# Performance work log

Hardware: AMD Instinct MI355X
Metric: run time of the kernel (lower is better)

Reference implementation:

```python
import jax, jax.numpy as jnp
import numpy as np

LEAKY_SLOPE = 0.2  # tf.nn.leaky_relu default alpha
NEG_INF = -1e9


def setup_inputs() -> dict:
    key = jax.random.key(0)
    k1, k2, k3, k4 = jax.random.split(key, 4)
    B, N, F, D, H = 1, 4096, 128, 64, 4
    features = jax.random.normal(k1, (B, N, F), dtype=jnp.float32)
    adj = jax.random.randint(k2, (N, N), 0, 2, dtype=jnp.int32)  # 0/1 adjacency
    W = jax.random.normal(k3, (H, F, D), dtype=jnp.float32) * 0.1
    attn_k = jax.random.normal(k4, (H, 2 * D, 1), dtype=jnp.float32) * 0.1
    return {"adj": adj, "features": features, "W": W, "attn_k": attn_k}


def reference(adj, features, W, attn_k):
    H, _, D = W.shape
    adj_f = adj.astype(jnp.float32)[None]       # [1, N, N], broadcast over batch
    mask = adj_f != 0.0
    outs = []
    for i in range(H):  # fixed small head loop (heads are structurally distinct weights)
        h = features @ W[i]                      # [B, N, D]
        a_self = h @ attn_k[i, :D]               # [B, N, 1]
        a_neigh = h @ attn_k[i, D:]              # [B, N, 1]
        scores = a_self + jnp.swapaxes(a_neigh, 1, 2)  # [B, N, N] additive scores
        scores = jax.nn.leaky_relu(scores, LEAKY_SLOPE)
        scores = jnp.where(mask, scores, NEG_INF)
        attn = jax.nn.softmax(scores, axis=-1)   # [B, N, N]
        outs.append((attn * adj_f) @ h)          # [B, N, D]
    out = jnp.concatenate(outs, axis=-1) if H > 1 else outs[0]
    return jax.nn.relu(out)
```

## Files before the change

kernel.cpp:

```cpp
#include <hip/hip_runtime.h>
#include <math.h>

#define NN 4096
#define FF 128
#define DD 64
#define HH 4
#define NC 256

typedef _Float16 f16x8 __attribute__((ext_vector_type(8)));
typedef _Float16 f16x2 __attribute__((ext_vector_type(2)));
typedef float    f32x4 __attribute__((ext_vector_type(4)));

__global__ __launch_bounds__(256) void adjbits_kernel(
    const int* __restrict__ adj, unsigned int* __restrict__ adjw)
{
    const int row  = blockIdx.x;
    const int wv   = threadIdx.x >> 6;
    const int lane = threadIdx.x & 63;
    for (int c = wv; c < 64; c += 4) {
        int a = adj[(size_t)row * NN + c * 64 + lane];
        unsigned long long m = __ballot(a != 0);
        if (lane == 0) {
            adjw[row * 128 + c * 2]     = (unsigned int)m;
            adjw[row * 128 + c * 2 + 1] = (unsigned int)(m >> 32);
        }
    }
}

__global__ __launch_bounds__(256) void prep_kernel(
    const float* __restrict__ feats, const float* __restrict__ W,
    const float* __restrict__ ak, _Float16* __restrict__ Ht,
    _Float16* __restrict__ Es, _Float16* __restrict__ Fs,
    _Float16* __restrict__ En, _Float16* __restrict__ Fn)
{
    __shared__ float Wt[64 * 132];
    __shared__ float ft[32 * 128];
    __shared__ float hlds[32 * 65];
    const int t  = threadIdx.x;
    const int h  = blockIdx.y;
    const int n0 = blockIdx.x * 32;

    {
        const float* Wh = W + h * (FF * DD);
        #pragma unroll
        for (int j = 0; j < 8; ++j) {
            int idx = j * 256 + t;
            int f   = idx >> 4;
            int d4  = idx & 15;
            float4 v = ((const float4*)Wh)[idx];
            Wt[(d4 * 4 + 0) * 132 + f] = v.x;
            Wt[(d4 * 4 + 1) * 132 + f] = v.y;
            Wt[(d4 * 4 + 2) * 132 + f] = v.z;
            Wt[(d4 * 4 + 3) * 132 + f] = v.w;
        }
        #pragma unroll
        for (int j = 0; j < 4; ++j) {
            int idx = j * 256 + t;
            int r = idx >> 5, f4 = idx & 31;
            ((float4*)ft)[r * 32 + f4] = ((const float4*)feats)[(size_t)(n0 + r) * 32 + f4];
        }
    }
    __syncthreads();

    const int d   = t & 63;
    const int wid = t >> 6;
    float acc[8];
    #pragma unroll
    for (int j = 0; j < 8; ++j) acc[j] = 0.f;

    for (int f4 = 0; f4 < 32; ++f4) {
        const float4 w4 = *(const float4*)&Wt[d * 132 + f4 * 4];
        #pragma unroll
        for (int j = 0; j < 8; ++j) {
            const int r = wid + 4 * j;
            const float4 fv = *(const float4*)&ft[r * 128 + f4 * 4];
            acc[j] += fv.x * w4.x + fv.y * w4.y + fv.z * w4.z + fv.w * w4.w;
        }
    }

    const float aks = ak[h * 128 + d];
    const float akn = ak[h * 128 + 64 + d];
    #pragma unroll
    for (int j = 0; j < 8; ++j) {
        const int r = wid + 4 * j;
        const float hv = acc[j];
        hlds[r * 65 + d] = hv;
        float v1 = hv * aks;
        float v2 = hv * akn;
        #pragma unroll
        for (int m = 32; m >= 1; m >>= 1) {
            v1 += __shfl_xor(v1, m, 64);
            v2 += __shfl_xor(v2, m, 64);
        }
        if (d == 0) {
            Es[h * NN + n0 + r] = (_Float16)__expf(v1);
            Fs[h * NN + n0 + r] = (_Float16)__expf(0.2f * v1);
            En[h * NN + n0 + r] = (_Float16)__expf(v2);
            Fn[h * NN + n0 + r] = (_Float16)__expf(0.2f * v2);
        }
    }
    __syncthreads();

    const int d2 = t >> 2;
    const int mq = (t & 3) * 8;
    f16x8 v;
    #pragma unroll
    for (int i = 0; i < 8; ++i) v[i] = (_Float16)hlds[(mq + i) * 65 + d2];
    *(f16x8*)(Ht + (size_t)(h * 64 + d2) * NN + n0 + mq) = v;
}

__global__ __launch_bounds__(256, 4) void attn_kernel(
    const unsigned int* __restrict__ adjw, const _Float16* __restrict__ Ht,
    const _Float16* __restrict__ Es, const _Float16* __restrict__ Fs,
    const _Float16* __restrict__ En, const _Float16* __restrict__ Fn,
    float* __restrict__ pacc, float* __restrict__ pden, int ksplit)
{
    __shared__ _Float16 Blds[2 * 64 * 32];

    const int t  = threadIdx.x;
    const int w  = t >> 6;
    const int l  = t & 63;
    const int lr = l & 15;
    const int kg = l >> 4;
    const int h  = blockIdx.y;
    const int s  = blockIdx.z;
    const int n0 = blockIdx.x * 128 + w * 32;
    const int mstart = s * ksplit;
    const int nchunk = ksplit >> 5;

    const int sd = t >> 2;
    const int sg = (t & 3) ^ (sd & 3);
    const _Float16* __restrict__ hstage = Ht + (size_t)(h * 64 + sd) * NN + sg * 8;
    const int swoff = sd * 32 + (t & 3) * 8;
    const int slot8 = (kg ^ (lr & 3)) * 8;

    const _Float16 es0 = Es[h * NN + n0 + lr],      fs0 = Fs[h * NN + n0 + lr];
    const _Float16 es1 = Es[h * NN + n0 + 16 + lr], fs1 = Fs[h * NN + n0 + 16 + lr];
    const f16x2 es20 = {es0, es0}, fs20 = {fs0, fs0};
    const f16x2 es21 = {es1, es1}, fs21 = {fs1, fs1};

    const _Float16* __restrict__ EnB = En + (size_t)h * NN;
    const _Float16* __restrict__ FnB = Fn + (size_t)h * NN;
    const int row0 = n0 + lr, row1 = n0 + 16 + lr;
    const int wb   = mstart >> 5;

    f32x4 acc[2][4] = {};
    f32x4 dacc[2]   = {};
    f16x8 ones;
    #pragma unroll
    for (int j = 0; j < 8; ++j) ones[j] = (_Float16)1.0f;

    union U8 { f16x8 v; unsigned int u[4]; };

    uint4 sreg = *(const uint4*)(hstage + mstart);

    for (int cq = 0; cq < (nchunk >> 2); ++cq) {
        const uint4 mk0 = *(const uint4*)&adjw[(size_t)row0 * 128 + wb + cq * 4];
        const uint4 mk1 = *(const uint4*)&adjw[(size_t)row1 * 128 + wb + cq * 4];

        #pragma unroll
        for (int ci = 0; ci < 4; ++ci) {
            const int c  = cq * 4 + ci;
            const int m0 = mstart + c * 32;
            const int buf = (ci & 1) * 2048;

            *(uint4*)&Blds[buf + swoff] = sreg;
            __syncthreads();

            {
                const int mn = (c + 1 < nchunk) ? m0 + 32 : m0;
                sreg = *(const uint4*)(hstage + mn);
            }

            const uint4 enq = *(const uint4*)(EnB + m0 + kg * 8);
            const uint4 fnq = *(const uint4*)(FnB + m0 + kg * 8);
            const unsigned int b0 =
                (ci == 0 ? mk0.x : ci == 1 ? mk0.y : ci == 2 ? mk0.z : mk0.w) >> (kg * 8);
            const unsigned int b1 =
                (ci == 0 ? mk1.x : ci == 1 ? mk1.y : ci == 2 ? mk1.z : mk1.w) >> (kg * 8);

            U8 A0, A1;
            #pragma unroll
            for (int p = 0; p < 4; ++p) {
                const unsigned int eu = p == 0 ? enq.x : p == 1 ? enq.y : p == 2 ? enq.z : enq.w;
                const unsigned int fu = p == 0 ? fnq.x : p == 1 ? fnq.y : p == 2 ? fnq.z : fnq.w;
                const f16x2 en2 = __builtin_bit_cast(f16x2, eu);
                const f16x2 fn2 = __builtin_bit_cast(f16x2, fu);
                const f16x2 v0 = __builtin_elementwise_max(es20 * en2, fs20 * fn2);
                const f16x2 v1 = __builtin_elementwise_max(es21 * en2, fs21 * fn2);
                const unsigned int mm0 = (((b0 >> (2 * p)) & 1u) ? 0x0000FFFFu : 0u)
                                       | (((b0 >> (2 * p + 1)) & 1u) ? 0xFFFF0000u : 0u);
                const unsigned int mm1 = (((b1 >> (2 * p)) & 1u) ? 0x0000FFFFu : 0u)
                                       | (((b1 >> (2 * p + 1)) & 1u) ? 0xFFFF0000u : 0u);
                A0.u[p] = __builtin_bit_cast(unsigned int, v0) & mm0;
                A1.u[p] = __builtin_bit_cast(unsigned int, v1) & mm1;
            }

            #pragma unroll
            for (int cb = 0; cb < 4; ++cb) {
                const f16x8 Bf = *(const f16x8*)&Blds[buf + (cb * 16 + lr) * 32 + slot8];
                acc[0][cb] = __builtin_amdgcn_mfma_f32_16x16x32_f16(A0.v, Bf, acc[0][cb], 0, 0, 0);
                acc[1][cb] = __builtin_amdgcn_mfma_f32_16x16x32_f16(A1.v, Bf, acc[1][cb], 0, 0, 0);
            }
            dacc[0] = __builtin_amdgcn_mfma_f32_16x16x32_f16(A0.v, ones, dacc[0], 0, 0, 0);
            dacc[1] = __builtin_amdgcn_mfma_f32_16x16x32_f16(A1.v, ones, dacc[1], 0, 0, 0);

            __syncthreads();
        }
    }

    #pragma unroll
    for (int rb = 0; rb < 2; ++rb) {
        #pragma unroll
        for (int r = 0; r < 4; ++r) {
            const int row = n0 + rb * 16 + kg * 4 + r;
            #pragma unroll
            for (int cb = 0; cb < 4; ++cb)
                pacc[((size_t)(s * NN + row)) * NC + h * 64 + cb * 16 + lr] = acc[rb][cb][r];
            if (lr == 0)
                pden[(s * NN + row) * 4 + h] = dacc[rb][r];
        }
    }
}

__global__ __launch_bounds__(256) void finalize_kernel(
    const float* __restrict__ pacc, const float* __restrict__ pden,
    float* __restrict__ out, int nsplit)
{
    const int n = blockIdx.x;
    const int c = threadIdx.x;
    float a = 0.f, d = 0.f;
    for (int s = 0; s < nsplit; ++s) {
        a += pacc[((size_t)(s * NN + n)) * NC + c];
        d += pden[(s * NN + n) * 4 + (c >> 6)];
    }
    const float o = (d > 0.f) ? a / d : 0.f;
    out[(size_t)n * NC + c] = o > 0.f ? o : 0.f;
}

extern "C" void kernel_launch(void* const* d_in, const int* in_sizes, int n_in,
                              void* d_out, int out_size, void* d_ws, size_t ws_size,
                              hipStream_t stream)
{
    const int*   adj   = (const int*)d_in[0];
    const float* feats = (const float*)d_in[1];
    const float* W     = (const float*)d_in[2];
    const float* ak    = (const float*)d_in[3];
    float*       out   = (float*)d_out;

    char* ws = (char*)d_ws;
    unsigned int* adjw = (unsigned int*)ws;
    _Float16*     Ht   = (_Float16*)(ws + (2ull << 20));
    _Float16*     Es   = (_Float16*)(ws + (4ull << 20));
    _Float16*     Fs   = (_Float16*)(ws + (4ull << 20) + (1 << 16));
    _Float16*     En   = (_Float16*)(ws + (4ull << 20) + (2 << 16));
    _Float16*     Fn   = (_Float16*)(ws + (4ull << 20) + (3 << 16));
    float*        pden = (float*)(ws + (4ull << 20) + (4 << 16));
    float*        pacc = (float*)(ws + (5ull << 20));

    int nsplit = 8;
    while (nsplit > 1 && ws_size < (5ull << 20) + (size_t)nsplit * (4ull << 20))
        nsplit >>= 1;
    const int ksplit = NN / nsplit;

    adjbits_kernel<<<NN, 256, 0, stream>>>(adj, adjw);
    prep_kernel<<<dim3(128, 4), 256, 0, stream>>>(feats, W, ak, Ht, Es, Fs, En, Fn);
    attn_kernel<<<dim3(32, 4, nsplit), 256, 0, stream>>>(adjw, Ht, Es, Fs, En, Fn, pacc, pden, ksplit);
    finalize_kernel<<<NN, 256, 0, stream>>>(pacc, pden, out, nsplit);
}
```

Baseline: 67.34 us.

## Pre-pack H in MFMA fragment layout and load B directly into registers

The prep kernel now writes H in a pre-swizzled per-32-row-chunk layout that matches the MFMA B-operand fragment, so the attention kernel can load B straight from global memory into registers. This removes the shared-memory staging and both __syncthreads per chunk. Each block is now a single wavefront, and B fragments are double-buffered in registers by software prefetch. The change also raises MFMA issue priority around the math and uses nontemporal stores for the partial sums, at the cost of more register pressure and each wave fetching B on its own rather than sharing it through LDS.

Result: slower. 70.25 us (+4.3%).

```diff
diff --git a/kernel.cpp b/kernel.cpp
--- a/kernel.cpp
+++ b/kernel.cpp
@@ -29,7 +29,7 @@
 
 __global__ __launch_bounds__(256) void prep_kernel(
     const float* __restrict__ feats, const float* __restrict__ W,
-    const float* __restrict__ ak, _Float16* __restrict__ Ht,
+    const float* __restrict__ ak, _Float16* __restrict__ Bpack,
     _Float16* __restrict__ Es, _Float16* __restrict__ Fs,
     _Float16* __restrict__ En, _Float16* __restrict__ Fn)
 {
@@ -101,38 +101,33 @@
     }
     __syncthreads();
 
-    const int d2 = t >> 2;
-    const int mq = (t & 3) * 8;
+    const int cb = t >> 6;
+    const int l  = t & 63;
+    const int lr = l & 15;
+    const int kg = l >> 4;
     f16x8 v;
     #pragma unroll
-    for (int i = 0; i < 8; ++i) v[i] = (_Float16)hlds[(mq + i) * 65 + d2];
-    *(f16x8*)(Ht + (size_t)(h * 64 + d2) * NN + n0 + mq) = v;
-}
-
-__global__ __launch_bounds__(256, 4) void attn_kernel(
-    const unsigned int* __restrict__ adjw, const _Float16* __restrict__ Ht,
+    for (int j = 0; j < 8; ++j)
+        v[j] = (_Float16)hlds[(kg * 8 + j) * 65 + cb * 16 + lr];
+    *(f16x8*)(Bpack + ((size_t)(h * 128 + blockIdx.x)) * 2048 + (cb * 64 + l) * 8) = v;
+}
+
+__global__ __launch_bounds__(64, 4) void attn_kernel(
+    const unsigned int* __restrict__ adjw, const _Float16* __restrict__ Bpack,
     const _Float16* __restrict__ Es, const _Float16* __restrict__ Fs,
     const _Float16* __restrict__ En, const _Float16* __restrict__ Fn,
     float* __restrict__ pacc, float* __restrict__ pden, int ksplit)
 {
-    __shared__ _Float16 Blds[2 * 64 * 32];
-
-    const int t  = threadIdx.x;
-    const int w  = t >> 6;
-    const int l  = t & 63;
+    const int l  = threadIdx.x;
     const int lr = l & 15;
     const int kg = l >> 4;
     const int h  = blockIdx.y;
+    const int n0 = blockIdx.x * 32;
     const int s  = blockIdx.z;
-    const int n0 = blockIdx.x * 128 + w * 32;
+
     const int mstart = s * ksplit;
     const int nchunk = ksplit >> 5;
-
-    const int sd = t >> 2;
-    const int sg = (t & 3) ^ (sd & 3);
-    const _Float16* __restrict__ hstage = Ht + (size_t)(h * 64 + sd) * NN + sg * 8;
-    const int swoff = sd * 32 + (t & 3) * 8;
-    const int slot8 = (kg ^ (lr & 3)) * 8;
+    const int wb     = mstart >> 5;
 
     const _Float16 es0 = Es[h * NN + n0 + lr],      fs0 = Fs[h * NN + n0 + lr];
     const _Float16 es1 = Es[h * NN + n0 + 16 + lr], fs1 = Fs[h * NN + n0 + 16 + lr];
@@ -142,7 +137,9 @@
     const _Float16* __restrict__ EnB = En + (size_t)h * NN;
     const _Float16* __restrict__ FnB = Fn + (size_t)h * NN;
     const int row0 = n0 + lr, row1 = n0 + 16 + lr;
-    const int wb   = mstart >> 5;
+
+    const _Float16* __restrict__ bp =
+        Bpack + ((size_t)(h * 128) + (mstart >> 5)) * 2048 + l * 8;
 
     f32x4 acc[2][4] = {};
     f32x4 dacc[2]   = {};
@@ -152,62 +149,67 @@
 
     union U8 { f16x8 v; unsigned int u[4]; };
 
-    uint4 sreg = *(const uint4*)(hstage + mstart);
+    f16x8 B_0[4], B_1[4];
+
+#define LOADB(DST, CIDX) do {                                                 \
+        int _c = (CIDX); _c = _c < nchunk ? _c : nchunk - 1;                  \
+        const _Float16* _b = bp + (size_t)_c * 2048;                          \
+        _Pragma("unroll")                                                     \
+        for (int _cb = 0; _cb < 4; ++_cb)                                     \
+            DST[_cb] = *(const f16x8*)(_b + _cb * 512);                       \
+    } while (0)
+
+#define STEP(BREG, C, MW0, MW1) do {                                          \
+        const int _m0 = mstart + (C) * 32;                                    \
+        const uint4 enq = *(const uint4*)(EnB + _m0 + kg * 8);                \
+        const uint4 fnq = *(const uint4*)(FnB + _m0 + kg * 8);                \
+        const unsigned int b0 = (MW0) >> (kg * 8);                            \
+        const unsigned int b1 = (MW1) >> (kg * 8);                            \
+        U8 A0, A1;                                                            \
+        _Pragma("unroll")                                                     \
+        for (int p = 0; p < 4; ++p) {                                         \
+            const unsigned int eu = p == 0 ? enq.x : p == 1 ? enq.y : p == 2 ? enq.z : enq.w; \
+            const unsigned int fu = p == 0 ? fnq.x : p == 1 ? fnq.y : p == 2 ? fnq.z : fnq.w; \
+            const f16x2 en2 = __builtin_bit_cast(f16x2, eu);                  \
+            const f16x2 fn2 = __builtin_bit_cast(f16x2, fu);                  \
+            const f16x2 v0 = __builtin_elementwise_max(es20 * en2, fs20 * fn2); \
+            const f16x2 v1 = __builtin_elementwise_max(es21 * en2, fs21 * fn2); \
+            const unsigned int mm0 = (((b0 >> (2 * p)) & 1u) ? 0x0000FFFFu : 0u) \
+                                   | (((b0 >> (2 * p + 1)) & 1u) ? 0xFFFF0000u : 0u); \
+            const unsigned int mm1 = (((b1 >> (2 * p)) & 1u) ? 0x0000FFFFu : 0u) \
+                                   | (((b1 >> (2 * p + 1)) & 1u) ? 0xFFFF0000u : 0u); \
+            A0.u[p] = __builtin_bit_cast(unsigned int, v0) & mm0;             \
+            A1.u[p] = __builtin_bit_cast(unsigned int, v1) & mm1;             \
+        }                                                                     \
+        __builtin_amdgcn_s_setprio(1);                                        \
+        _Pragma("unroll")                                                     \
+        for (int _cb = 0; _cb < 4; ++_cb) {                                   \
+            acc[0][_cb] = __builtin_amdgcn_mfma_f32_16x16x32_f16(A0.v, BREG[_cb], acc[0][_cb], 0, 0, 0); \
+            acc[1][_cb] = __builtin_amdgcn_mfma_f32_16x16x32_f16(A1.v, BREG[_cb], acc[1][_cb], 0, 0, 0); \
+        }                                                                     \
+        dacc[0] = __builtin_amdgcn_mfma_f32_16x16x32_f16(A0.v, ones, dacc[0], 0, 0, 0); \
+        dacc[1] = __builtin_amdgcn_mfma_f32_16x16x32_f16(A1.v, ones, dacc[1], 0, 0, 0); \
+        __builtin_amdgcn_s_setprio(0);                                        \
+    } while (0)
+
+    LOADB(B_0, 0);
 
     for (int cq = 0; cq < (nchunk >> 2); ++cq) {
-        const uint4 mk0 = *(const uint4*)&adjw[(size_t)row0 * 128 + wb + cq * 4];
-        const uint4 mk1 = *(const uint4*)&adjw[(size_t)row1 * 128 + wb + cq * 4];
-
-        #pragma unroll
-        for (int ci = 0; ci < 4; ++ci) {
-            const int c  = cq * 4 + ci;
-            const int m0 = mstart + c * 32;
-            const int buf = (ci & 1) * 2048;
-
-            *(uint4*)&Blds[buf + swoff] = sreg;
-            __syncthreads();
-
-            {
-                const int mn = (c + 1 < nchunk) ? m0 + 32 : m0;
-                sreg = *(const uint4*)(hstage + mn);
-            }
-
-            const uint4 enq = *(const uint4*)(EnB + m0 + kg * 8);
-            const uint4 fnq = *(const uint4*)(FnB + m0 + kg * 8);
-            const unsigned int b0 =
-                (ci == 0 ? mk0.x : ci == 1 ? mk0.y : ci == 2 ? mk0.z : mk0.w) >> (kg * 8);
-            const unsigned int b1 =
-                (ci == 0 ? mk1.x : ci == 1 ? mk1.y : ci == 2 ? mk1.z : mk1.w) >> (kg * 8);
-
-            U8 A0, A1;
-            #pragma unroll
-            for (int p = 0; p < 4; ++p) {
-                const unsigned int eu = p == 0 ? enq.x : p == 1 ? enq.y : p == 2 ? enq.z : enq.w;
-                const unsigned int fu = p == 0 ? fnq.x : p == 1 ? fnq.y : p == 2 ? fnq.z : fnq.w;
-                const f16x2 en2 = __builtin_bit_cast(f16x2, eu);
-                const f16x2 fn2 = __builtin_bit_cast(f16x2, fu);
-                const f16x2 v0 = __builtin_elementwise_max(es20 * en2, fs20 * fn2);
-                const f16x2 v1 = __builtin_elementwise_max(es21 * en2, fs21 * fn2);
-                const unsigned int mm0 = (((b0 >> (2 * p)) & 1u) ? 0x0000FFFFu : 0u)
-                                       | (((b0 >> (2 * p + 1)) & 1u) ? 0xFFFF0000u : 0u);
-                const unsigned int mm1 = (((b1 >> (2 * p)) & 1u) ? 0x0000FFFFu : 0u)
-                                       | (((b1 >> (2 * p + 1)) & 1u) ? 0xFFFF0000u : 0u);
-                A0.u[p] = __builtin_bit_cast(unsigned int, v0) & mm0;
-                A1.u[p] = __builtin_bit_cast(unsigned int, v1) & mm1;
-            }
-
-            #pragma unroll
-            for (int cb = 0; cb < 4; ++cb) {
-                const f16x8 Bf = *(const f16x8*)&Blds[buf + (cb * 16 + lr) * 32 + slot8];
-                acc[0][cb] = __builtin_amdgcn_mfma_f32_16x16x32_f16(A0.v, Bf, acc[0][cb], 0, 0, 0);
-                acc[1][cb] = __builtin_amdgcn_mfma_f32_16x16x32_f16(A1.v, Bf, acc[1][cb], 0, 0, 0);
-            }
-            dacc[0] = __builtin_amdgcn_mfma_f32_16x16x32_f16(A0.v, ones, dacc[0], 0, 0, 0);
-            dacc[1] = __builtin_amdgcn_mfma_f32_16x16x32_f16(A1.v, ones, dacc[1], 0, 0, 0);
-
-            __syncthreads();
-        }
-    }
+        const int c0 = cq * 4;
+        const uint4 mk0 = *(const uint4*)&adjw[(size_t)row0 * 128 + wb + c0];
+        const uint4 mk1 = *(const uint4*)&adjw[(size_t)row1 * 128 + wb + c0];
+
+        LOADB(B_1, c0 + 1);
+        STEP(B_0, c0 + 0, mk0.x, mk1.x);
+        LOADB(B_0, c0 + 2);
+        STEP(B_1, c0 + 1, mk0.y, mk1.y);
+        LOADB(B_1, c0 + 3);
+        STEP(B_0, c0 + 2, mk0.z, mk1.z);
+        LOADB(B_0, c0 + 4);
+        STEP(B_1, c0 + 3, mk0.w, mk1.w);
+    }
+#undef LOADB
+#undef STEP
 
     #pragma unroll
     for (int rb = 0; rb < 2; ++rb) {
@@ -215,8 +217,11 @@
         for (int r = 0; r < 4; ++r) {
             const int row = n0 + rb * 16 + kg * 4 + r;
             #pragma unroll
-            for (int cb = 0; cb < 4; ++cb)
-                pacc[((size_t)(s * NN + row)) * NC + h * 64 + cb * 16 + lr] = acc[rb][cb][r];
+            for (int cb = 0; cb < 4; ++cb) {
+                float4 vv = {acc[rb][cb][r], 0.f, 0.f, 0.f};
+                __builtin_nontemporal_store(acc[rb][cb][r],
+                    &pacc[((size_t)(s * NN + row)) * NC + h * 64 + cb * 16 + lr]);
+            }
             if (lr == 0)
                 pden[(s * NN + row) * 4 + h] = dacc[rb][r];
         }
@@ -249,14 +254,14 @@
     float*       out   = (float*)d_out;
 
     char* ws = (char*)d_ws;
-    unsigned int* adjw = (unsigned int*)ws;
-    _Float16*     Ht   = (_Float16*)(ws + (2ull << 20));
-    _Float16*     Es   = (_Float16*)(ws + (4ull << 20));
-    _Float16*     Fs   = (_Float16*)(ws + (4ull << 20) + (1 << 16));
-    _Float16*     En   = (_Float16*)(ws + (4ull << 20) + (2 << 16));
-    _Float16*     Fn   = (_Float16*)(ws + (4ull << 20) + (3 << 16));
-    float*        pden = (float*)(ws + (4ull << 20) + (4 << 16));
-    float*        pacc = (float*)(ws + (5ull << 20));
+    unsigned int* adjw  = (unsigned int*)ws;
+    _Float16*     Bpack = (_Float16*)(ws + (2ull << 20));
+    _Float16*     Es    = (_Float16*)(ws + (4ull << 20));
+    _Float16*     Fs    = (_Float16*)(ws + (4ull << 20) + (1 << 16));
+    _Float16*     En    = (_Float16*)(ws + (4ull << 20) + (2 << 16));
+    _Float16*     Fn    = (_Float16*)(ws + (4ull << 20) + (3 << 16));
+    float*        pden  = (float*)(ws + (4ull << 20) + (4 << 16));
+    float*        pacc  = (float*)(ws + (5ull << 20));
 
     int nsplit = 8;
     while (nsplit > 1 && ws_size < (5ull << 20) + (size_t)nsplit * (4ull << 20))
@@ -264,7 +269,7 @@
     const int ksplit = NN / nsplit;
 
     adjbits_kernel<<<NN, 256, 0, stream>>>(adj, adjw);
-    prep_kernel<<<dim3(128, 4), 256, 0, stream>>>(feats, W, ak, Ht, Es, Fs, En, Fn);
-    attn_kernel<<<dim3(32, 4, nsplit), 256, 0, stream>>>(adjw, Ht, Es, Fs, En, Fn, pacc, pden, ksplit);
+    prep_kernel<<<dim3(128, 4), 256, 0, stream>>>(feats, W, ak, Bpack, Es, Fs, En, Fn);
+    attn_kernel<<<dim3(128, 4, nsplit), 64, 0, stream>>>(adjw, Bpack, Es, Fs, En, Fn, pacc, pden, ksplit);
     finalize_kernel<<<NN, 256, 0, stream>>>(pacc, pden, out, nsplit);
 }
```

## Merge adjacency and projection prep, pre-pack MFMA B tiles, deepen attention pipeline

Applied to the files above, without the earlier changes.

Merges the adjacency bit-packing and feature projection kernels into one launch so there is one fewer launch and the two can overlap. The projected features are now stored pre-packed in MFMA operand order, so the attention kernel copies tiles contiguously into LDS without swizzled transposed loads. The attention loop prefetches B two chunks ahead and En/Fn one chunk ahead, and drops one barrier per chunk. It also rotates the chunk start per block to spread memory traffic, raises wave priority around the MFMAs, and writes partial sums with nontemporal stores. The cost is more live registers and a more intricate double-buffer schedule, which may lower occupancy.

Measured after the change: 93.60 us. +39.0%, slower.

```diff
diff --git a/kernel.cpp b/kernel.cpp
--- a/kernel.cpp
+++ b/kernel.cpp
@@ -11,34 +11,36 @@
 typedef _Float16 f16x2 __attribute__((ext_vector_type(2)));
 typedef float    f32x4 __attribute__((ext_vector_type(4)));
 
-__global__ __launch_bounds__(256) void adjbits_kernel(
-    const int* __restrict__ adj, unsigned int* __restrict__ adjw)
-{
-    const int row  = blockIdx.x;
-    const int wv   = threadIdx.x >> 6;
-    const int lane = threadIdx.x & 63;
-    for (int c = wv; c < 64; c += 4) {
-        int a = adj[(size_t)row * NN + c * 64 + lane];
-        unsigned long long m = __ballot(a != 0);
-        if (lane == 0) {
-            adjw[row * 128 + c * 2]     = (unsigned int)m;
-            adjw[row * 128 + c * 2 + 1] = (unsigned int)(m >> 32);
-        }
-    }
-}
-
-__global__ __launch_bounds__(256) void prep_kernel(
-    const float* __restrict__ feats, const float* __restrict__ W,
-    const float* __restrict__ ak, _Float16* __restrict__ Ht,
+__global__ __launch_bounds__(256) void prep_adj_kernel(
+    const int* __restrict__ adj, const float* __restrict__ feats,
+    const float* __restrict__ W, const float* __restrict__ ak,
+    unsigned int* __restrict__ adjw, _Float16* __restrict__ Bpack,
     _Float16* __restrict__ Es, _Float16* __restrict__ Fs,
     _Float16* __restrict__ En, _Float16* __restrict__ Fn)
 {
+    const int t = threadIdx.x;
+
+    if (blockIdx.x >= 512) {
+        const int row  = blockIdx.x - 512;
+        const int wv   = t >> 6;
+        const int lane = t & 63;
+        for (int c = wv; c < 64; c += 4) {
+            int a = adj[(size_t)row * NN + c * 64 + lane];
+            unsigned long long m = __ballot(a != 0);
+            if (lane == 0) {
+                adjw[row * 128 + c * 2]     = (unsigned int)m;
+                adjw[row * 128 + c * 2 + 1] = (unsigned int)(m >> 32);
+            }
+        }
+        return;
+    }
+
     __shared__ float Wt[64 * 132];
     __shared__ float ft[32 * 128];
     __shared__ float hlds[32 * 65];
-    const int t  = threadIdx.x;
-    const int h  = blockIdx.y;
-    const int n0 = blockIdx.x * 32;
+    const int h  = blockIdx.x & 3;
+    const int tile = blockIdx.x >> 2;
+    const int n0 = tile * 32;
 
     {
         const float* Wh = W + h * (FF * DD);
@@ -101,21 +103,24 @@
     }
     __syncthreads();
 
-    const int d2 = t >> 2;
-    const int mq = (t & 3) * 8;
+    const int cb = t >> 6;
+    const int l  = t & 63;
+    const int lr = l & 15;
+    const int kg = l >> 4;
     f16x8 v;
     #pragma unroll
-    for (int i = 0; i < 8; ++i) v[i] = (_Float16)hlds[(mq + i) * 65 + d2];
-    *(f16x8*)(Ht + (size_t)(h * 64 + d2) * NN + n0 + mq) = v;
+    for (int j = 0; j < 8; ++j)
+        v[j] = (_Float16)hlds[(kg * 8 + j) * 65 + cb * 16 + lr];
+    *(f16x8*)(Bpack + ((size_t)(h * 128 + tile)) * 2048 + (cb * 64 + l) * 8) = v;
 }
 
 __global__ __launch_bounds__(256, 4) void attn_kernel(
-    const unsigned int* __restrict__ adjw, const _Float16* __restrict__ Ht,
+    const unsigned int* __restrict__ adjw, const _Float16* __restrict__ Bpack,
     const _Float16* __restrict__ Es, const _Float16* __restrict__ Fs,
     const _Float16* __restrict__ En, const _Float16* __restrict__ Fn,
     float* __restrict__ pacc, float* __restrict__ pden, int ksplit)
 {
-    __shared__ _Float16 Blds[2 * 64 * 32];
+    __shared__ _Float16 Blds[2][2048];
 
     const int t  = threadIdx.x;
     const int w  = t >> 6;
@@ -125,14 +130,14 @@
     const int h  = blockIdx.y;
     const int s  = blockIdx.z;
     const int n0 = blockIdx.x * 128 + w * 32;
+
     const int mstart = s * ksplit;
     const int nchunk = ksplit >> 5;
-
-    const int sd = t >> 2;
-    const int sg = (t & 3) ^ (sd & 3);
-    const _Float16* __restrict__ hstage = Ht + (size_t)(h * 64 + sd) * NN + sg * 8;
-    const int swoff = sd * 32 + (t & 3) * 8;
-    const int slot8 = (kg ^ (lr & 3)) * 8;
+    const int ncq    = nchunk >> 2;
+    const int coff   = blockIdx.x & (ncq - 1);
+    const int wb     = mstart >> 5;
+
+#define PC(c) (((((c) >> 2) + coff) & (ncq - 1)) * 4 + ((c) & 3))
 
     const _Float16 es0 = Es[h * NN + n0 + lr],      fs0 = Fs[h * NN + n0 + lr];
     const _Float16 es1 = Es[h * NN + n0 + 16 + lr], fs1 = Fs[h * NN + n0 + 16 + lr];
@@ -142,7 +147,9 @@
     const _Float16* __restrict__ EnB = En + (size_t)h * NN;
     const _Float16* __restrict__ FnB = Fn + (size_t)h * NN;
     const int row0 = n0 + lr, row1 = n0 + 16 + lr;
-    const int wb   = mstart >> 5;
+
+    const _Float16* __restrict__ bp =
+        Bpack + ((size_t)(h * 128) + wb) * 2048 + t * 8;
 
     f32x4 acc[2][4] = {};
     f32x4 dacc[2]   = {};
@@ -152,38 +159,45 @@
 
     union U8 { f16x8 v; unsigned int u[4]; };
 
-    uint4 sreg = *(const uint4*)(hstage + mstart);
-
-    for (int cq = 0; cq < (nchunk >> 2); ++cq) {
-        const uint4 mk0 = *(const uint4*)&adjw[(size_t)row0 * 128 + wb + cq * 4];
-        const uint4 mk1 = *(const uint4*)&adjw[(size_t)row1 * 128 + wb + cq * 4];
+    uint4 sreg = *(const uint4*)(bp + (size_t)PC(0) * 2048);
+    *(uint4*)&Blds[0][t * 8] = sreg;
+    sreg = *(const uint4*)(bp + (size_t)PC(1) * 2048);
+    uint4 enqc = *(const uint4*)(EnB + mstart + PC(0) * 32 + kg * 8);
+    uint4 fnqc = *(const uint4*)(FnB + mstart + PC(0) * 32 + kg * 8);
+    __syncthreads();
+
+    for (int cq = 0; cq < ncq; ++cq) {
+        const int cqp = (cq + coff) & (ncq - 1);
+        const uint4 mk0 = *(const uint4*)&adjw[(size_t)row0 * 128 + wb + cqp * 4];
+        const uint4 mk1 = *(const uint4*)&adjw[(size_t)row1 * 128 + wb + cqp * 4];
 
         #pragma unroll
         for (int ci = 0; ci < 4; ++ci) {
-            const int c  = cq * 4 + ci;
-            const int m0 = mstart + c * 32;
-            const int buf = (ci & 1) * 2048;
-
-            *(uint4*)&Blds[buf + swoff] = sreg;
-            __syncthreads();
-
+            const int c = cq * 4 + ci;
+
+            uint4 nreg;
             {
-                const int mn = (c + 1 < nchunk) ? m0 + 32 : m0;
-                sreg = *(const uint4*)(hstage + mn);
-            }
-
-            const uint4 enq = *(const uint4*)(EnB + m0 + kg * 8);
-            const uint4 fnq = *(const uint4*)(FnB + m0 + kg * 8);
+                const int cn = (c + 2 < nchunk) ? c + 2 : c;
+                nreg = *(const uint4*)(bp + (size_t)PC(cn) * 2048);
+            }
+            if (c + 1 < nchunk)
+                *(uint4*)&Blds[(c + 1) & 1][t * 8] = sreg;
+            uint4 enq_n, fnq_n;
+            {
+                const int cn = (c + 1 < nchunk) ? c + 1 : c;
+                enq_n = *(const uint4*)(EnB + mstart + PC(cn) * 32 + kg * 8);
+                fnq_n = *(const uint4*)(FnB + mstart + PC(cn) * 32 + kg * 8);
+            }
+
             const unsigned int b0 =
                 (ci == 0 ? mk0.x : ci == 1 ? mk0.y : ci == 2 ? mk0.z : mk0.w) >> (kg * 8);
             const unsigned int b1 =
                 (ci == 0 ? mk1.x : ci == 1 ? mk1.y : ci == 2 ? mk1.z : mk1.w) >> (kg * 8);
-
             U8 A0, A1;
             #pragma unroll
             for (int p = 0; p < 4; ++p) {
-                const unsigned int eu = p == 0 ? enq.x : p == 1 ? enq.y : p == 2 ? enq.z : enq.w;
-                const unsigned int fu = p == 0 ? fnq.x : p == 1 ? fnq.y : p == 2 ? fnq.z : fnq.w;
+                const unsigned int eu = p == 0 ? enqc.x : p == 1 ? enqc.y : p == 2 ? enqc.z : enqc.w;
+                const unsigned int fu = p == 0 ? fnqc.x : p == 1 ? fnqc.y : p == 2 ? fnqc.z : fnqc.w;
                 const f16x2 en2 = __builtin_bit_cast(f16x2, eu);
                 const f16x2 fn2 = __builtin_bit_cast(f16x2, fu);
                 const f16x2 v0 = __builtin_elementwise_max(es20 * en2, fs20 * fn2);
@@ -196,18 +210,24 @@
                 A1.u[p] = __builtin_bit_cast(unsigned int, v1) & mm1;
             }
 
+            __builtin_amdgcn_s_setprio(1);
             #pragma unroll
             for (int cb = 0; cb < 4; ++cb) {
-                const f16x8 Bf = *(const f16x8*)&Blds[buf + (cb * 16 + lr) * 32 + slot8];
+                const f16x8 Bf = *(const f16x8*)&Blds[c & 1][(cb * 64 + l) * 8];
                 acc[0][cb] = __builtin_amdgcn_mfma_f32_16x16x32_f16(A0.v, Bf, acc[0][cb], 0, 0, 0);
                 acc[1][cb] = __builtin_amdgcn_mfma_f32_16x16x32_f16(A1.v, Bf, acc[1][cb], 0, 0, 0);
             }
             dacc[0] = __builtin_amdgcn_mfma_f32_16x16x32_f16(A0.v, ones, dacc[0], 0, 0, 0);
             dacc[1] = __builtin_amdgcn_mfma_f32_16x16x32_f16(A1.v, ones, dacc[1], 0, 0, 0);
+            __builtin_amdgcn_s_setprio(0);
 
             __syncthreads();
-        }
-    }
+            sreg = nreg;
+            enqc = enq_n;
+            fnqc = fnq_n;
+        }
+    }
+#undef PC
 
     #pragma unroll
     for (int rb = 0; rb < 2; ++rb) {
@@ -216,7 +236,8 @@
             const int row = n0 + rb * 16 + kg * 4 + r;
             #pragma unroll
             for (int cb = 0; cb < 4; ++cb)
-                pacc[((size_t)(s * NN + row)) * NC + h * 64 + cb * 16 + lr] = acc[rb][cb][r];
+                __builtin_nontemporal_store(acc[rb][cb][r],
+                    &pacc[((size_t)(s * NN + row)) * NC + h * 64 + cb * 16 + lr]);
             if (lr == 0)
                 pden[(s * NN + row) * 4 + h] = dacc[rb][r];
         }
@@ -249,22 +270,23 @@
     float*       out   = (float*)d_out;
 
     char* ws = (char*)d_ws;
-    unsigned int* adjw = (unsigned int*)ws;
-    _Float16*     Ht   = (_Float16*)(ws + (2ull << 20));
-    _Float16*     Es   = (_Float16*)(ws + (4ull << 20));
-    _Float16*     Fs   = (_Float16*)(ws + (4ull << 20) + (1 << 16));
-    _Float16*     En   = (_Float16*)(ws + (4ull << 20) + (2 << 16));
-    _Float16*     Fn   = (_Float16*)(ws + (4ull << 20) + (3 << 16));
-    float*        pden = (float*)(ws + (4ull << 20) + (4 << 16));
-    float*        pacc = (float*)(ws + (5ull << 20));
+    unsigned int* adjw  = (unsigned int*)ws;
+    _Float16*     Bpack = (_Float16*)(ws + (2ull << 20));
+    _Float16*     Es    = (_Float16*)(ws + (4ull << 20));
+    _Float16*     Fs    = (_Float16*)(ws + (4ull << 20) + (1 << 16));
+    _Float16*     En    = (_Float16*)(ws + (4ull << 20) + (2 << 16));
+    _Float16*     Fn    = (_Float16*)(ws + (4ull << 20) + (3 << 16));
+    float*        pden  = (float*)(ws + (4ull << 20) + (4 << 16));
+    float*        pacc  = (float*)(ws + (5ull << 20));
 
     int nsplit = 8;
     while (nsplit > 1 && ws_size < (5ull << 20) + (size_t)nsplit * (4ull << 20))
         nsplit >>= 1;
     const int ksplit = NN / nsplit;
 
-    adjbits_kernel<<<NN, 256, 0, stream>>>(adj, adjw);
-    prep_kernel<<<dim3(128, 4), 256, 0, stream>>>(feats, W, ak, Ht, Es, Fs, En, Fn);
-    attn_kernel<<<dim3(32, 4, nsplit), 256, 0, stream>>>(adjw, Ht, Es, Fs, En, Fn, pacc, pden, ksplit);
+    prep_adj_kernel<<<512 + NN, 256, 0, stream>>>(adj, feats, W, ak, adjw,
+                                                  Bpack, Es, Fs, En, Fn);
+    attn_kernel<<<dim3(32, 4, nsplit), 256, 0, stream>>>(adjw, Bpack, Es, Fs, En, Fn,
+                                                         pacc, pden, ksplit);
     finalize_kernel<<<NN, 256, 0, stream>>>(pacc, pden, out, nsplit);
 }
```
